# Kernel tuning notes

Measured on AMD Instinct MI355X. Metric: run time of the kernel, lower is better.

## Reference

```python
import jax, jax.numpy as jnp
import numpy as np

N = 50000
E = 1_600_000
D_IN = 128
D_H = 64
D_E = 32
NEG_SLOPE = 0.2


def setup_inputs() -> dict:
    key = jax.random.key(0)
    ks = jax.random.split(key, 20)
    p = lambda k, sh: jax.random.normal(k, sh, jnp.float32) * 0.1
    return {
        "x": jax.random.normal(ks[0], (N, D_IN), jnp.float32),
        "edge_index": jax.random.randint(ks[1], (2, E), 0, N, jnp.int32),
        "edge_attr": jax.random.normal(ks[2], (E, D_E), jnp.float32),
        # layer 1 params (GATv2Conv, heads=1)
        "Wl1": p(ks[3], (D_IN, D_H)), "bl1": p(ks[4], (D_H,)),
        "Wr1": p(ks[5], (D_IN, D_H)), "br1": p(ks[6], (D_H,)),
        "We1": p(ks[7], (D_E, D_H)),
        "att1": p(ks[8], (D_H,)), "bias1": p(ks[9], (D_H,)),
        # layer 2 params
        "Wl2": p(ks[10], (D_H, D_H)), "bl2": p(ks[11], (D_H,)),
        "Wr2": p(ks[12], (D_H, D_H)), "br2": p(ks[13], (D_H,)),
        "We2": p(ks[14], (D_E, D_H)),
        "att2": p(ks[15], (D_H,)), "bias2": p(ks[16], (D_H,)),
        # classifier
        "Wc": p(ks[17], (D_H, 2)), "bc": p(ks[18], (2,)),
    }


def _gatv2(x, src, dst, eattr, Wl, bl, Wr, br, We, att, bias, n):
    # x: [n, d_in]; src/dst: [Ea]; eattr: [Ea, d_e]
    xl = x @ Wl + bl                      # [n, d_h] (source transform; also message value)
    xr = x @ Wr + br                      # [n, d_h] (target transform)
    z = xl[src] + xr[dst] + eattr @ We    # [Ea, d_h]
    score = jax.nn.leaky_relu(z, NEG_SLOPE) @ att  # [Ea]
    # numerically stable softmax over incoming edges per destination node
    m = jax.ops.segment_max(score, dst, num_segments=n)
    ex = jnp.exp(score - m[dst])
    denom = jax.ops.segment_sum(ex, dst, num_segments=n)
    alpha = ex / denom[dst]               # [Ea]
    out = jax.ops.segment_sum(alpha[:, None] * xl[src], dst, num_segments=n)
    return out + bias


def reference(x, edge_index, edge_attr,
              Wl1, bl1, Wr1, br1, We1, att1, bias1,
              Wl2, bl2, Wr2, br2, We2, att2, bias2,
              Wc, bc):
    n = x.shape[0]
    src, dst = edge_index[0], edge_index[1]
    # add self-loops with fill_value='mean' (PyG default with edge_attr):
    # self-loop edge feature of node i = mean of edge_attr over edges into i
    e = edge_attr.shape[0]
    deg = jax.ops.segment_sum(jnp.ones((e,), edge_attr.dtype), dst, num_segments=n)
    loop_attr = jax.ops.segment_sum(edge_attr, dst, num_segments=n) / jnp.maximum(deg, 1.0)[:, None]
    loop = jnp.arange(n, dtype=edge_index.dtype)
    src_a = jnp.concatenate([src, loop])
    dst_a = jnp.concatenate([dst, loop])
    ea = jnp.concatenate([edge_attr, loop_attr], axis=0)

    h = jax.nn.relu(_gatv2(x, src_a, dst_a, ea, Wl1, bl1, Wr1, br1, We1, att1, bias1, n))
    # dropout(p=0.2) is identity in eval mode
    h = jax.nn.relu(_gatv2(h, src_a, dst_a, ea, Wl2, bl2, Wr2, br2, We2, att2, bias2, n))
    return h @ Wc + bc  # [n, 2]
```

## Files before the change

kernel.cpp:

```cpp
#include <hip/hip_runtime.h>
#include <hip/hip_bf16.h>

#define NEG_SLOPE 0.2f

__device__ __forceinline__ float bf2f(unsigned short u) {
    return __uint_as_float((unsigned)u << 16);
}
__device__ __forceinline__ float bflo(unsigned u) { return __uint_as_float(u << 16); }
__device__ __forceinline__ float bfhi(unsigned u) { return __uint_as_float(u & 0xFFFF0000u); }
__device__ __forceinline__ unsigned short f2bf(float f) {
    unsigned b = __float_as_uint(f);
    return (unsigned short)((b + 0x7FFFu + ((b >> 16) & 1u)) >> 16);
}

__global__ void k_hist(const int* __restrict__ dst, int E, int* __restrict__ deg) {
    int e = blockIdx.x * 256 + threadIdx.x;
    if (e < E) atomicAdd(&deg[dst[e]], 1);
}

__global__ __launch_bounds__(1024) void k_scan_chunk(const int* __restrict__ deg,
                                                     int* __restrict__ start,
                                                     int* __restrict__ csum, int n) {
    __shared__ int wsum[16];
    const int lane = threadIdx.x & 63;
    const int w = threadIdx.x >> 6;
    int i = blockIdx.x * 1024 + (int)threadIdx.x;
    int v = (i < n) ? deg[i] : 0;
    int s = v;
#pragma unroll
    for (int o = 1; o < 64; o <<= 1) {
        int u = __shfl_up(s, o);
        if (lane >= o) s += u;
    }
    if (lane == 63) wsum[w] = s;
    __syncthreads();
    if (w == 0) {
        int ws = (lane < 16) ? wsum[lane] : 0;
#pragma unroll
        for (int o = 1; o < 16; o <<= 1) {
            int u = __shfl_up(ws, o);
            if (lane >= o) ws += u;
        }
        if (lane < 16) wsum[lane] = ws;
    }
    __syncthreads();
    int woff = (w == 0) ? 0 : wsum[w - 1];
    int incl = s + woff;
    if (i < n) start[i] = incl - v;
    if (threadIdx.x == 1023) csum[blockIdx.x] = incl;
}

__global__ void k_scan_top(int* __restrict__ csum, int nch, int* __restrict__ start, int n) {
    int t = threadIdx.x;
    int v = (t < nch) ? csum[t] : 0;
    int s = v;
#pragma unroll
    for (int o = 1; o < 64; o <<= 1) {
        int u = __shfl_up(s, o);
        if (t >= o) s += u;
    }
    if (t < nch) csum[t] = s - v;
    if (t == 63) start[n] = s;
}

__global__ void k_scan_apply(int* __restrict__ start, const int* __restrict__ csum, int n) {
    int i = blockIdx.x * 256 + threadIdx.x;
    if (i < n) start[i] += csum[i >> 10];
}

__global__ void k_fill(const int* __restrict__ src, const int* __restrict__ dst, int E,
                       const int* __restrict__ start, int* __restrict__ cursor,
                       int* __restrict__ perm, int* __restrict__ src_sorted,
                       int* __restrict__ sortpos) {
    int e = blockIdx.x * 256 + threadIdx.x;
    if (e >= E) return;
    int d = dst[e];
    int idx = start[d] + atomicAdd(&cursor[d], 1);
    perm[idx] = e;
    src_sorted[idx] = src[e];
    sortpos[e] = idx;
}

__global__ __launch_bounds__(256) void k_loop_csr(
    const float* __restrict__ eattr, const int* __restrict__ perm,
    const int* __restrict__ start, float* __restrict__ loop_attr, int n) {
    int node = blockIdx.x * 4 + (threadIdx.x >> 6);
    int t = threadIdx.x & 63;
    if (node >= n) return;
    int a = start[node], b = start[node + 1];
    int g = t >> 3, gl = t & 7;
    float4 acc = make_float4(0.f, 0.f, 0.f, 0.f);
    int j = a + g;
    for (; j + 8 < b; j += 16) {
        int e1 = perm[j];
        int e2 = perm[j + 8];
        const float4 v1 = *(const float4*)&eattr[(size_t)e1 * 32 + gl * 4];
        const float4 v2 = *(const float4*)&eattr[(size_t)e2 * 32 + gl * 4];
        acc.x += v1.x + v2.x; acc.y += v1.y + v2.y;
        acc.z += v1.z + v2.z; acc.w += v1.w + v2.w;
    }
    if (j < b) {
        int e = perm[j];
        const float4 v = *(const float4*)&eattr[(size_t)e * 32 + gl * 4];
        acc.x += v.x; acc.y += v.y; acc.z += v.z; acc.w += v.w;
    }
#pragma unroll
    for (int mask = 8; mask <= 32; mask <<= 1) {
        acc.x += __shfl_xor(acc.x, mask);
        acc.y += __shfl_xor(acc.y, mask);
        acc.z += __shfl_xor(acc.z, mask);
        acc.w += __shfl_xor(acc.w, mask);
    }
    if (t < 8) {
        float deg = fmaxf((float)(b - a), 1.f);
        float4 o = make_float4(acc.x / deg, acc.y / deg, acc.z / deg, acc.w / deg);
        *(float4*)&loop_attr[(size_t)node * 32 + gl * 4] = o;
    }
}

template <int DIN>
__global__ void k_node_transform(const float* __restrict__ h,
                                 const float* __restrict__ Wl, const float* __restrict__ bl,
                                 const float* __restrict__ Wr, const float* __restrict__ br,
                                 unsigned short* __restrict__ xlb,
                                 unsigned short* __restrict__ xrb, int n) {
    __shared__ float hs[4][DIN];
    int node0 = blockIdx.x * 4;
    int tid = threadIdx.x;
    for (int idx = tid; idx < 4 * DIN; idx += 256) {
        int ln = idx / DIN, k = idx % DIN;
        int node = node0 + ln;
        hs[ln][k] = (node < n) ? h[(long long)node * DIN + k] : 0.f;
    }
    __syncthreads();
    int ln = tid >> 6;
    int j = tid & 63;
    int node = node0 + ln;
    if (node >= n) return;
    float al = bl[j], ar = br[j];
#pragma unroll 8
    for (int k = 0; k < DIN; ++k) {
        float hv = hs[ln][k];
        al += hv * Wl[k * 64 + j];
        ar += hv * Wr[k * 64 + j];
    }
    xlb[(long long)node * 64 + j] = f2bf(al);
    xrb[(long long)node * 64 + j] = f2bf(ar);
}

__global__ __launch_bounds__(256, 2) void k_edge_score(
    const unsigned short* __restrict__ xlb, const unsigned short* __restrict__ xrb,
    const float* __restrict__ eattr,
    const float* __restrict__ We, const float* __restrict__ att,
    const int* __restrict__ src, const int* __restrict__ dst,
    const int* __restrict__ sortpos, int E,
    float* __restrict__ ex_sorted) {
    __shared__ __align__(16) float We_s[32 * 64];
    __shared__ __align__(16) float ea_T[32][132];
    __shared__ float att_s[64];
    __shared__ int s_s[128], d_s[128], sp_s[128];

    const int tid = threadIdx.x;
    const int ge0 = blockIdx.x * 128;

    if (tid < 128) {
        int ge = ge0 + tid;
        bool ok = ge < E;
        s_s[tid] = ok ? src[ge] : 0;
        d_s[tid] = ok ? dst[ge] : 0;
        sp_s[tid] = ok ? sortpos[ge] : 0;
    }
    {
        const int e = tid & 127;
        const int kc = (tid >> 7) * 16;
        const int ge = ge0 + e;
        float4 a = make_float4(0.f, 0.f, 0.f, 0.f), b = a, c = a, d4 = a;
        if (ge < E) {
            const float4* p = (const float4*)(eattr + (size_t)ge * 32 + kc);
            a = p[0]; b = p[1]; c = p[2]; d4 = p[3];
        }
        ea_T[kc + 0][e] = a.x;  ea_T[kc + 1][e] = a.y;  ea_T[kc + 2][e] = a.z;  ea_T[kc + 3][e] = a.w;
        ea_T[kc + 4][e] = b.x;  ea_T[kc + 5][e] = b.y;  ea_T[kc + 6][e] = b.z;  ea_T[kc + 7][e] = b.w;
        ea_T[kc + 8][e] = c.x;  ea_T[kc + 9][e] = c.y;  ea_T[kc + 10][e] = c.z; ea_T[kc + 11][e] = c.w;
        ea_T[kc + 12][e] = d4.x; ea_T[kc + 13][e] = d4.y; ea_T[kc + 14][e] = d4.z; ea_T[kc + 15][e] = d4.w;
    }
    for (int i = tid; i < 2048; i += 256) We_s[i] = We[i];
    if (tid < 64) att_s[tid] = att[tid];
    __syncthreads();

    const int w = tid >> 6, l = tid & 63;
    const int t0 = (l & 15) * 4;
    const int e0 = w * 32 + (l >> 4) * 8;

    ushort4 xlv[8], xrv[8];
#pragma unroll
    for (int j = 0; j < 8; ++j) {
        const int eb = e0 + j;
        xlv[j] = *(const ushort4*)&xlb[(size_t)s_s[eb] * 64 + t0];
        xrv[j] = *(const ushort4*)&xrb[(size_t)d_s[eb] * 64 + t0];
    }

    float z[8][4];
#pragma unroll
    for (int j = 0; j < 8; ++j)
#pragma unroll
        for (int i = 0; i < 4; ++i) z[j][i] = 0.f;

#pragma unroll 4
    for (int k = 0; k < 32; ++k) {
        const float4 ev0 = *(const float4*)&ea_T[k][e0];
        const float4 ev1 = *(const float4*)&ea_T[k][e0 + 4];
        const float4 wv = *(const float4*)&We_s[k * 64 + t0];
        const float ee[8] = {ev0.x, ev0.y, ev0.z, ev0.w, ev1.x, ev1.y, ev1.z, ev1.w};
        const float ww[4] = {wv.x, wv.y, wv.z, wv.w};
#pragma unroll
        for (int j = 0; j < 8; ++j)
#pragma unroll
            for (int i = 0; i < 4; ++i) z[j][i] += ee[j] * ww[i];
    }

    const float4 av = *(const float4*)&att_s[t0];
    const float aa[4] = {av.x, av.y, av.z, av.w};
    float v[8];
#pragma unroll
    for (int j = 0; j < 8; ++j) {
        const float xll[4] = {bf2f(xlv[j].x), bf2f(xlv[j].y), bf2f(xlv[j].z), bf2f(xlv[j].w)};
        const float xrr[4] = {bf2f(xrv[j].x), bf2f(xrv[j].y), bf2f(xrv[j].z), bf2f(xrv[j].w)};
        float acc = 0.f;
#pragma unroll
        for (int i = 0; i < 4; ++i) {
            float zz = z[j][i] + xll[i] + xrr[i];
            zz = (zz > 0.f) ? zz : NEG_SLOPE * zz;
            acc += aa[i] * zz;
        }
        v[j] = acc;
    }
#pragma unroll
    for (int m = 1; m < 16; m <<= 1) {
#pragma unroll
        for (int j = 0; j < 8; ++j) v[j] += __shfl_xor(v[j], m);
    }
    if ((l & 15) == 0) {
#pragma unroll
        for (int j = 0; j < 8; ++j) {
            int ge = ge0 + e0 + j;
            if (ge < E) ex_sorted[sp_s[e0 + j]] = __expf(v[j]);
        }
    }
}

template <bool FINAL>
__global__ __launch_bounds__(256, 2) void k_node_aggr(
    const unsigned short* __restrict__ xlb, const unsigned short* __restrict__ xrb,
    const float* __restrict__ loop_attr,
    const float* __restrict__ We, const float* __restrict__ att,
    const int* __restrict__ start,
    const int* __restrict__ src_sorted, const float* __restrict__ ex_sorted,
    const float* __restrict__ bias,
    const float* __restrict__ Wc, const float* __restrict__ bc,
    float* __restrict__ hout, int n) {
    __shared__ float la_s[4][32];
    const int ln = threadIdx.x >> 6;
    const int node = blockIdx.x * 4 + ln;
    const int t = threadIdx.x & 63;

    if (threadIdx.x < 128) {
        int nn = blockIdx.x * 4 + (threadIdx.x >> 5);
        int k = threadIdx.x & 31;
        la_s[threadIdx.x >> 5][k] = (nn < n) ? loop_attr[(size_t)nn * 32 + k] : 0.f;
    }
    __syncthreads();
    if (node >= n) return;

    float exl;
    {
        float zl = bf2f(xlb[(size_t)node * 64 + t]) + bf2f(xrb[(size_t)node * 64 + t]);
#pragma unroll 8
        for (int k = 0; k < 32; ++k) zl += We[k * 64 + t] * la_s[ln][k];
        zl = (zl > 0.f) ? zl : NEG_SLOPE * zl;
        float v = att[t] * zl;
#pragma unroll
        for (int mask = 1; mask <= 32; mask <<= 1) v += __shfl_xor(v, mask);
        exl = __expf(v);
    }

    const int g = t >> 3;
    const int c8 = t & 7;
    int a = start[node], b = start[node + 1];

    float acc[8] = {0.f, 0.f, 0.f, 0.f, 0.f, 0.f, 0.f, 0.f};
    float den = 0.f;
    if (g == 0) {
        const uint4 q = *(const uint4*)&xlb[(size_t)node * 64 + c8 * 8];
        acc[0] = exl * bflo(q.x); acc[1] = exl * bfhi(q.x);
        acc[2] = exl * bflo(q.y); acc[3] = exl * bfhi(q.y);
        acc[4] = exl * bflo(q.z); acc[5] = exl * bfhi(q.z);
        acc[6] = exl * bflo(q.w); acc[7] = exl * bfhi(q.w);
        den = exl;
    }
    for (int j = a; j < b; j += 64) {
        int m = b - j; if (m > 64) m = 64;
        int sj = 0; float exj = 0.f;
        if (t < m) { sj = src_sorted[j + t]; exj = ex_sorted[j + t]; }
        for (int i = 0; i < m; i += 16) {
            const int i0 = i + g, i1 = i + 8 + g;
            const int s0 = __shfl(sj, i0); const float e0 = __shfl(exj, i0);
            const int s1 = __shfl(sj, i1); const float e1 = __shfl(exj, i1);
            uint4 q0 = *(const uint4*)&xlb[(size_t)s0 * 64 + c8 * 8];
            uint4 q1 = *(const uint4*)&xlb[(size_t)s1 * 64 + c8 * 8];
            if (i0 < m) {
                acc[0] += e0 * bflo(q0.x); acc[1] += e0 * bfhi(q0.x);
                acc[2] += e0 * bflo(q0.y); acc[3] += e0 * bfhi(q0.y);
                acc[4] += e0 * bflo(q0.z); acc[5] += e0 * bfhi(q0.z);
                acc[6] += e0 * bflo(q0.w); acc[7] += e0 * bfhi(q0.w);
                den += e0;
            }
            if (i1 < m) {
                acc[0] += e1 * bflo(q1.x); acc[1] += e1 * bfhi(q1.x);
                acc[2] += e1 * bflo(q1.y); acc[3] += e1 * bfhi(q1.y);
                acc[4] += e1 * bflo(q1.z); acc[5] += e1 * bfhi(q1.z);
                acc[6] += e1 * bflo(q1.w); acc[7] += e1 * bfhi(q1.w);
                den += e1;
            }
        }
    }
#pragma unroll
    for (int mask = 8; mask <= 32; mask <<= 1) {
#pragma unroll
        for (int r = 0; r < 8; ++r) acc[r] += __shfl_xor(acc[r], mask);
        den += __shfl_xor(den, mask);
    }
    if (!FINAL) {
        if (g == 0) {
            float h[8];
#pragma unroll
            for (int r = 0; r < 8; ++r)
                h[r] = fmaxf(acc[r] / den + bias[c8 * 8 + r], 0.f);
            float4 o0 = make_float4(h[0], h[1], h[2], h[3]);
            float4 o1 = make_float4(h[4], h[5], h[6], h[7]);
            *(float4*)&hout[(size_t)node * 64 + c8 * 8] = o0;
            *(float4*)&hout[(size_t)node * 64 + c8 * 8 + 4] = o1;
        }
    } else {
        float v0 = 0.f, v1 = 0.f;
        if (g == 0) {
#pragma unroll
            for (int r = 0; r < 8; ++r) {
                const int ch = c8 * 8 + r;
                const float h = fmaxf(acc[r] / den + bias[ch], 0.f);
                v0 += h * Wc[ch * 2 + 0];
                v1 += h * Wc[ch * 2 + 1];
            }
        }
#pragma unroll
        for (int mask = 1; mask <= 4; mask <<= 1) {
            v0 += __shfl_xor(v0, mask);
            v1 += __shfl_xor(v1, mask);
        }
        if (t == 0) {
            hout[(size_t)node * 2 + 0] = v0 + bc[0];
            hout[(size_t)node * 2 + 1] = v1 + bc[1];
        }
    }
}

extern "C" void kernel_launch(void* const* d_in, const int* in_sizes, int n_in,
                              void* d_out, int out_size, void* d_ws, size_t ws_size,
                              hipStream_t stream) {
    const float* x     = (const float*)d_in[0];
    const int*   ei    = (const int*)d_in[1];
    const float* eattr = (const float*)d_in[2];
    const float* Wl1 = (const float*)d_in[3];
    const float* bl1 = (const float*)d_in[4];
    const float* Wr1 = (const float*)d_in[5];
    const float* br1 = (const float*)d_in[6];
    const float* We1 = (const float*)d_in[7];
    const float* att1 = (const float*)d_in[8];
    const float* bias1 = (const float*)d_in[9];
    const float* Wl2 = (const float*)d_in[10];
    const float* bl2 = (const float*)d_in[11];
    const float* Wr2 = (const float*)d_in[12];
    const float* br2 = (const float*)d_in[13];
    const float* We2 = (const float*)d_in[14];
    const float* att2 = (const float*)d_in[15];
    const float* bias2 = (const float*)d_in[16];
    const float* Wc = (const float*)d_in[17];
    const float* bc = (const float*)d_in[18];

    const int N = in_sizes[0] / 128;
    const int E = in_sizes[1] / 2;
    const int* src = ei;
    const int* dst = ei + E;

    char* w = (char*)d_ws;
    auto alloc = [&](size_t bytes) {
        char* p = w;
        w += (bytes + 255) & ~(size_t)255;
        return p;
    };
    unsigned short* xlb        = (unsigned short*)alloc((size_t)N * 64 * 2);
    unsigned short* xrb        = (unsigned short*)alloc((size_t)N * 64 * 2);
    float*          hbuf       = (float*)alloc((size_t)N * 64 * 4);
    float*          loop_attr  = (float*)alloc((size_t)N * 32 * 4);
    int*            deg_i      = (int*)alloc((size_t)N * 4);
    int*            start      = (int*)alloc((size_t)(N + 1) * 4);
    int*            cursor     = (int*)alloc((size_t)N * 4);
    int*            csum       = (int*)alloc(256 * 4);
    int*            perm       = (int*)alloc((size_t)E * 4);
    int*            src_sorted = (int*)alloc((size_t)E * 4);
    int*            sortpos    = (int*)alloc((size_t)E * 4);
    float*          ex_sorted  = (float*)alloc((size_t)E * 4);

    const int THREADS = 256;
    const int score_blocks = (E + 127) / 128;
    const int node4_blocks = (N + 3) / 4;
    const int edge_blocks = (E + THREADS - 1) / THREADS;
    const int nchunks = (N + 1023) / 1024;

    hipMemsetAsync(deg_i, 0, (size_t)N * 4, stream);
    hipMemsetAsync(cursor, 0, (size_t)N * 4, stream);
    k_hist<<<edge_blocks, THREADS, 0, stream>>>(dst, E, deg_i);
    k_scan_chunk<<<nchunks, 1024, 0, stream>>>(deg_i, start, csum, N);
    k_scan_top<<<1, 64, 0, stream>>>(csum, nchunks, start, N);
    k_scan_apply<<<(N + THREADS - 1) / THREADS, THREADS, 0, stream>>>(start, csum, N);
    k_fill<<<edge_blocks, THREADS, 0, stream>>>(src, dst, E, start, cursor,
                                                perm, src_sorted, sortpos);
    k_loop_csr<<<node4_blocks, THREADS, 0, stream>>>(eattr, perm, start, loop_attr, N);

    k_node_transform<128><<<node4_blocks, THREADS, 0, stream>>>(x, Wl1, bl1, Wr1, br1,
                                                                xlb, xrb, N);
    k_edge_score<<<score_blocks, THREADS, 0, stream>>>(
        xlb, xrb, eattr, We1, att1, src, dst, sortpos, E, ex_sorted);
    k_node_aggr<false><<<node4_blocks, THREADS, 0, stream>>>(
        xlb, xrb, loop_attr, We1, att1, start, src_sorted, ex_sorted,
        bias1, Wc, bc, hbuf, N);

    k_node_transform<64><<<node4_blocks, THREADS, 0, stream>>>(hbuf, Wl2, bl2, Wr2, br2,
                                                               xlb, xrb, N);
    k_edge_score<<<score_blocks, THREADS, 0, stream>>>(
        xlb, xrb, eattr, We2, att2, src, dst, sortpos, E, ex_sorted);
    k_node_aggr<true><<<node4_blocks, THREADS, 0, stream>>>(
        xlb, xrb, loop_attr, We2, att2, start, src_sorted, ex_sorted,
        bias2, Wc, bc, (float*)d_out, N);
}
```

Measured before the change: 745.2 us.

## Compute edge-attribute projection in edge score kernel with bf16 MFMA

Replaces the scalar FP32 eattr@We inner product in the edge-score kernel with 16x16x32 bf16 MFMA instructions. Edge attributes are converted to bf16 and staged in LDS in fragment layout, and We is loaded directly into register fragments. The xl/xr gathers are reorganized into 16-byte loads that match the MFMA output layout, and the shared-memory index staging is dropped. This reduces ALU work and LDS usage, but rounds edge_attr and We to bf16, which adds error to the attention scores.

```diff
diff --git a/kernel.cpp b/kernel.cpp
--- a/kernel.cpp
+++ b/kernel.cpp
@@ -2,6 +2,9 @@
 #include <hip/hip_bf16.h>
 
 #define NEG_SLOPE 0.2f
+
+typedef __attribute__((ext_vector_type(8))) short bf16x8;
+typedef __attribute__((ext_vector_type(4))) float f32x4;
 
 __device__ __forceinline__ float bf2f(unsigned short u) {
     return __uint_as_float((unsigned)u << 16);
@@ -155,96 +158,115 @@
     const int* __restrict__ src, const int* __restrict__ dst,
     const int* __restrict__ sortpos, int E,
     float* __restrict__ ex_sorted) {
-    __shared__ __align__(16) float We_s[32 * 64];
-    __shared__ __align__(16) float ea_T[32][132];
-    __shared__ float att_s[64];
-    __shared__ int s_s[128], d_s[128], sp_s[128];
+    __shared__ __align__(16) short ea_frag[4][128][8];
 
     const int tid = threadIdx.x;
     const int ge0 = blockIdx.x * 128;
-
-    if (tid < 128) {
-        int ge = ge0 + tid;
+    const int w = tid >> 6, l = tid & 63;
+    const int lo16 = l & 15, hi4 = l >> 4;
+
+    int sq[2], dq[2];
+#pragma unroll
+    for (int et = 0; et < 2; ++et) {
+        int ge = ge0 + w * 32 + et * 16 + lo16;
         bool ok = ge < E;
-        s_s[tid] = ok ? src[ge] : 0;
-        d_s[tid] = ok ? dst[ge] : 0;
-        sp_s[tid] = ok ? sortpos[ge] : 0;
-    }
+        sq[et] = ok ? src[ge] : 0;
+        dq[et] = ok ? dst[ge] : 0;
+    }
+    uint4 xlg[2][2], xrg[2][2];
+#pragma unroll
+    for (int et = 0; et < 2; ++et) {
+        const size_t lbase = (size_t)sq[et] * 64 + hi4 * 16;
+        const size_t rbase = (size_t)dq[et] * 64 + hi4 * 16;
+        xlg[et][0] = *(const uint4*)&xlb[lbase];
+        xlg[et][1] = *(const uint4*)&xlb[lbase + 8];
+        xrg[et][0] = *(const uint4*)&xrb[rbase];
+        xrg[et][1] = *(const uint4*)&xrb[rbase + 8];
+    }
+
     {
         const int e = tid & 127;
-        const int kc = (tid >> 7) * 16;
+        const int c0 = (tid >> 7) * 2;
         const int ge = ge0 + e;
         float4 a = make_float4(0.f, 0.f, 0.f, 0.f), b = a, c = a, d4 = a;
         if (ge < E) {
-            const float4* p = (const float4*)(eattr + (size_t)ge * 32 + kc);
+            const float4* p = (const float4*)(eattr + (size_t)ge * 32 + c0 * 8);
             a = p[0]; b = p[1]; c = p[2]; d4 = p[3];
         }
-        ea_T[kc + 0][e] = a.x;  ea_T[kc + 1][e] = a.y;  ea_T[kc + 2][e] = a.z;  ea_T[kc + 3][e] = a.w;
-        ea_T[kc + 4][e] = b.x;  ea_T[kc + 5][e] = b.y;  ea_T[kc + 6][e] = b.z;  ea_T[kc + 7][e] = b.w;
-        ea_T[kc + 8][e] = c.x;  ea_T[kc + 9][e] = c.y;  ea_T[kc + 10][e] = c.z; ea_T[kc + 11][e] = c.w;
-        ea_T[kc + 12][e] = d4.x; ea_T[kc + 13][e] = d4.y; ea_T[kc + 14][e] = d4.z; ea_T[kc + 15][e] = d4.w;
-    }
-    for (int i = tid; i < 2048; i += 256) We_s[i] = We[i];
-    if (tid < 64) att_s[tid] = att[tid];
+        bf16x8 lo, hi;
+        lo[0] = (short)f2bf(a.x); lo[1] = (short)f2bf(a.y); lo[2] = (short)f2bf(a.z); lo[3] = (short)f2bf(a.w);
+        lo[4] = (short)f2bf(b.x); lo[5] = (short)f2bf(b.y); lo[6] = (short)f2bf(b.z); lo[7] = (short)f2bf(b.w);
+        hi[0] = (short)f2bf(c.x); hi[1] = (short)f2bf(c.y); hi[2] = (short)f2bf(c.z); hi[3] = (short)f2bf(c.w);
+        hi[4] = (short)f2bf(d4.x); hi[5] = (short)f2bf(d4.y); hi[6] = (short)f2bf(d4.z); hi[7] = (short)f2bf(d4.w);
+        *(bf16x8*)&ea_frag[c0 + 0][e][0] = lo;
+        *(bf16x8*)&ea_frag[c0 + 1][e][0] = hi;
+    }
+
+    bf16x8 afrag[4];
+#pragma unroll
+    for (int ct = 0; ct < 4; ++ct) {
+        const int ch = (lo16 >> 2) * 16 + ct * 4 + (lo16 & 3);
+#pragma unroll
+        for (int j = 0; j < 8; ++j) {
+            afrag[ct][j] = (short)f2bf(We[(hi4 * 8 + j) * 64 + ch]);
+        }
+    }
+    float attf[16];
+    {
+        const float4 a0 = *(const float4*)&att[hi4 * 16 + 0];
+        const float4 a1 = *(const float4*)&att[hi4 * 16 + 4];
+        const float4 a2 = *(const float4*)&att[hi4 * 16 + 8];
+        const float4 a3 = *(const float4*)&att[hi4 * 16 + 12];
+        attf[0] = a0.x;  attf[1] = a0.y;  attf[2] = a0.z;  attf[3] = a0.w;
+        attf[4] = a1.x;  attf[5] = a1.y;  attf[6] = a1.z;  attf[7] = a1.w;
+        attf[8] = a2.x;  attf[9] = a2.y;  attf[10] = a2.z; attf[11] = a2.w;
+        attf[12] = a3.x; attf[13] = a3.y; attf[14] = a3.z; attf[15] = a3.w;
+    }
     __syncthreads();
 
-    const int w = tid >> 6, l = tid & 63;
-    const int t0 = (l & 15) * 4;
-    const int e0 = w * 32 + (l >> 4) * 8;
-
-    ushort4 xlv[8], xrv[8];
-#pragma unroll
-    for (int j = 0; j < 8; ++j) {
-        const int eb = e0 + j;
-        xlv[j] = *(const ushort4*)&xlb[(size_t)s_s[eb] * 64 + t0];
-        xrv[j] = *(const ushort4*)&xrb[(size_t)d_s[eb] * 64 + t0];
-    }
-
-    float z[8][4];
-#pragma unroll
-    for (int j = 0; j < 8; ++j)
-#pragma unroll
-        for (int i = 0; i < 4; ++i) z[j][i] = 0.f;
-
-#pragma unroll 4
-    for (int k = 0; k < 32; ++k) {
-        const float4 ev0 = *(const float4*)&ea_T[k][e0];
-        const float4 ev1 = *(const float4*)&ea_T[k][e0 + 4];
-        const float4 wv = *(const float4*)&We_s[k * 64 + t0];
-        const float ee[8] = {ev0.x, ev0.y, ev0.z, ev0.w, ev1.x, ev1.y, ev1.z, ev1.w};
-        const float ww[4] = {wv.x, wv.y, wv.z, wv.w};
-#pragma unroll
-        for (int j = 0; j < 8; ++j)
-#pragma unroll
-            for (int i = 0; i < 4; ++i) z[j][i] += ee[j] * ww[i];
-    }
-
-    const float4 av = *(const float4*)&att_s[t0];
-    const float aa[4] = {av.x, av.y, av.z, av.w};
-    float v[8];
-#pragma unroll
-    for (int j = 0; j < 8; ++j) {
-        const float xll[4] = {bf2f(xlv[j].x), bf2f(xlv[j].y), bf2f(xlv[j].z), bf2f(xlv[j].w)};
-        const float xrr[4] = {bf2f(xrv[j].x), bf2f(xrv[j].y), bf2f(xrv[j].z), bf2f(xrv[j].w)};
-        float acc = 0.f;
-#pragma unroll
-        for (int i = 0; i < 4; ++i) {
-            float zz = z[j][i] + xll[i] + xrr[i];
-            zz = (zz > 0.f) ? zz : NEG_SLOPE * zz;
-            acc += aa[i] * zz;
-        }
-        v[j] = acc;
-    }
-#pragma unroll
-    for (int m = 1; m < 16; m <<= 1) {
-#pragma unroll
-        for (int j = 0; j < 8; ++j) v[j] += __shfl_xor(v[j], m);
-    }
-    if ((l & 15) == 0) {
-#pragma unroll
-        for (int j = 0; j < 8; ++j) {
-            int ge = ge0 + e0 + j;
-            if (ge < E) ex_sorted[sp_s[e0 + j]] = __expf(v[j]);
+    f32x4 acc[2][4];
+#pragma unroll
+    for (int et = 0; et < 2; ++et) {
+        bf16x8 bfrag = *(const bf16x8*)&ea_frag[hi4][w * 32 + et * 16 + lo16][0];
+#pragma unroll
+        for (int ct = 0; ct < 4; ++ct) {
+            f32x4 zero = {0.f, 0.f, 0.f, 0.f};
+            acc[et][ct] = __builtin_amdgcn_mfma_f32_16x16x32_bf16(afrag[ct], bfrag, zero, 0, 0, 0);
+        }
+    }
+
+#pragma unroll
+    for (int et = 0; et < 2; ++et) {
+        float xlf[16], xrf[16];
+#pragma unroll
+        for (int h = 0; h < 2; ++h) {
+            const uint4 ql = xlg[et][h];
+            const uint4 qr = xrg[et][h];
+            xlf[h * 8 + 0] = bflo(ql.x); xlf[h * 8 + 1] = bfhi(ql.x);
+            xlf[h * 8 + 2] = bflo(ql.y); xlf[h * 8 + 3] = bfhi(ql.y);
+            xlf[h * 8 + 4] = bflo(ql.z); xlf[h * 8 + 5] = bfhi(ql.z);
+            xlf[h * 8 + 6] = bflo(ql.w); xlf[h * 8 + 7] = bfhi(ql.w);
+            xrf[h * 8 + 0] = bflo(qr.x); xrf[h * 8 + 1] = bfhi(qr.x);
+            xrf[h * 8 + 2] = bflo(qr.y); xrf[h * 8 + 3] = bfhi(qr.y);
+            xrf[h * 8 + 4] = bflo(qr.z); xrf[h * 8 + 5] = bfhi(qr.z);
+            xrf[h * 8 + 6] = bflo(qr.w); xrf[h * 8 + 7] = bfhi(qr.w);
+        }
+        float part = 0.f;
+#pragma unroll
+        for (int ct = 0; ct < 4; ++ct) {
+#pragma unroll
+            for (int r = 0; r < 4; ++r) {
+                const int i = ct * 4 + r;
+                float zz = acc[et][ct][r] + xlf[i] + xrf[i];
+                zz = (zz > 0.f) ? zz : NEG_SLOPE * zz;
+                part += attf[i] * zz;
+            }
+        }
+        part += __shfl_xor(part, 16);
+        part += __shfl_xor(part, 32);
+        if (l < 16) {
+            int ge = ge0 + w * 32 + et * 16 + l;
+            if (ge < E) ex_sorted[sortpos[ge]] = __expf(part);
         }
     }
 }
```

After: 751.2 us. Within noise of the previous version (+0.8%).
